# Kernel tuning notes

Hardware: AMD Instinct MI355X
Metric: run time of the kernel (lower is better)

The kernel has to match this reference:

```python
import jax, jax.numpy as jnp
import numpy as np

W_H = 512
RING_WIDTH = 1
IN_F = 128
OUT_F = 128


def _ring_ids():
    # static ring assignment per pixel, mirrors torch module's self.r / ring_width bins
    ax = np.arange(-W_H / 2, W_H / 2, dtype=np.float64)
    x, y = np.meshgrid(ax, ax, indexing='ij')
    r = np.sqrt(x * x + y * y)
    ring = (r // RING_WIDTH).astype(np.int32).reshape(-1)  # [H*W]
    len_r = int(np.sqrt(2.0) * (W_H / 2)) + 1
    iter_r = len_r // RING_WIDTH + (1 if len_r % RING_WIDTH != 0 else 0)
    return jnp.asarray(ring), iter_r


def setup_inputs() -> dict:
    key = jax.random.key(0)
    ks = jax.random.split(key, 7)
    return {
        'image_re': jax.random.normal(ks[0], (W_H, W_H, IN_F), jnp.float32),
        'image_im': jax.random.normal(ks[1], (W_H, W_H, IN_F), jnp.float32),
        'mask': jax.random.randint(ks[2], (W_H, W_H), 0, 2).astype(jnp.int32),
        'output_re': jnp.zeros((W_H, W_H, OUT_F), jnp.float32),
        'output_im': jnp.zeros((W_H, W_H, OUT_F), jnp.float32),
        'w1_re': jax.random.normal(ks[3], (IN_F, OUT_F), jnp.float32),
        'w1_im': jax.random.normal(ks[4], (IN_F, OUT_F), jnp.float32),
        'w2_re': jax.random.normal(ks[5], (IN_F, OUT_F), jnp.float32),
        'w2_im': jax.random.normal(ks[6], (IN_F, OUT_F), jnp.float32),
    }


def reference(image_re, image_im, mask, output_re, output_im,
              w1_re, w1_im, w2_re, w2_im):
    ring, n_rings = _ring_ids()
    H, _, F_in = image_re.shape
    x_re = image_re.reshape(-1, F_in)  # [N, F_in]
    x_im = image_im.reshape(-1, F_in)
    m = mask.reshape(-1, 1)
    u = (m == 0).astype(x_re.dtype)  # uncorrupted indicator
    c = (m == 1).astype(x_re.dtype)  # corrupted indicator

    # uncor complex matmul (x*u) @ W1, as 4 real GEMMs
    xu_re, xu_im = x_re * u, x_im * u
    mm1_re = xu_re @ w1_re - xu_im @ w1_im
    mm1_im = xu_re @ w1_im + xu_im @ w1_re

    # per-ring mean of mm1 (denominator = full ring size, matching neighbor.shape[0])
    counts = jax.ops.segment_sum(jnp.ones((x_re.shape[0],), x_re.dtype), ring,
                                 num_segments=n_rings)
    denom = jnp.maximum(counts, 1.0)[:, None]
    sum_re = jax.ops.segment_sum(mm1_re, ring, num_segments=n_rings) / denom
    sum_im = jax.ops.segment_sum(mm1_im, ring, num_segments=n_rings) / denom
    sre = sum_re[ring]  # [N, F_out] per-pixel broadcast of its ring mean
    sim = sum_im[ring]

    # cor complex matmul (x*c) @ W2
    xc_re, xc_im = x_re * c, x_im * c
    mm2_re = xc_re @ w2_re - xc_im @ w2_im
    mm2_im = xc_re @ w2_im + xc_im @ w2_re

    out_re = u * (0.5 * (mm1_re + sre)) + c * (mm2_re - sre)
    out_im = u * (0.5 * (mm1_im + sim)) + c * (mm2_im - sim)
    # real/imag stacked on last axis -> [H, H, F_out, 2]
    return jnp.stack([out_re, out_im], axis=-1).reshape(H, H, -1, 2)
```

## Files before the change

kernel.cpp:

```cpp
#include <hip/hip_runtime.h>
#include <hip/hip_bf16.h>
#include <stdint.h>


#define WH 512
#define NPIX (WH * WH)
#define NF 128
#define NRINGS 363

typedef unsigned short u16;
typedef __attribute__((ext_vector_type(8))) short short8;
typedef __attribute__((ext_vector_type(4))) float floatx4;

__device__ __forceinline__ u16 f2bf(float x) {
    uint32_t u = __float_as_uint(x);
    uint32_t r = (u + 0x7FFFu + ((u >> 16) & 1u)) >> 16;
    return (u16)r;
}
__device__ __forceinline__ uint32_t pk(float a, float b) {
    return (uint32_t)f2bf(a) | ((uint32_t)f2bf(b) << 16);
}
__device__ __forceinline__ short8 negbf(short8 v) {
    union { short8 s; uint32_t u[4]; } x;
    x.s = v;
    x.u[0] ^= 0x80008000u; x.u[1] ^= 0x80008000u;
    x.u[2] ^= 0x80008000u; x.u[3] ^= 0x80008000u;
    return x.s;
}
__device__ __forceinline__ floatx4 mfma16(short8 a, short8 b, floatx4 c) {
    return __builtin_amdgcn_mfma_f32_16x16x32_bf16(a, b, c, 0, 0, 0);
}

__global__ void k_build_bt(const float* __restrict__ w1r, const float* __restrict__ w1i,
                           const float* __restrict__ w2r, const float* __restrict__ w2i,
                           u16* __restrict__ bt) {
    int n = blockIdx.x, k = threadIdx.x;
    int src = k * NF + n;
    float a1r = w1r[src], a1i = w1i[src], a2r = w2r[src], a2i = w2i[src];
    int d = n * NF + k;
    bt[0 * 16384 + d] = f2bf(a1r - a2r);
    bt[1 * 16384 + d] = f2bf(a2r);
    bt[2 * 16384 + d] = f2bf(a1i - a2i);
    bt[3 * 16384 + d] = f2bf(a2i);
}

#define BROW 40
#define LDS_AR 0
#define LDS_AI 5120
#define LDS_B  10240

__global__ __launch_bounds__(256, 2) void k_gemm(
    const float* __restrict__ xr, const float* __restrict__ xi,
    const int* __restrict__ mask, const u16* __restrict__ bt,
    float* __restrict__ out)
{
    __shared__ u16 lds[30720];
    const int t = threadIdx.x;
    const int pbase = blockIdx.x * 128;
    const int w = t >> 6, lane = t & 63;
    const int quad = lane >> 4, l16 = lane & 15;

    floatx4 accRe[2][8], accIm[2][8];
#pragma unroll
    for (int mi = 0; mi < 2; mi++)
#pragma unroll
        for (int ni = 0; ni < 8; ni++) {
            accRe[mi][ni] = (floatx4)0.0f;
            accIm[mi][ni] = (floatx4)0.0f;
        }

    bool uu[2];
    uu[0] = (mask[pbase + w * 32 + l16] == 0);
    uu[1] = (mask[pbase + w * 32 + 16 + l16] == 0);

    const int sr = t >> 1, sh = t & 1;
    const float4* xr4 = (const float4*)(xr + (size_t)(pbase + sr) * NF);
    const float4* xi4 = (const float4*)(xi + (size_t)(pbase + sr) * NF);

    for (int kw = 0; kw < 4; kw++) {
        if (kw) __syncthreads();
        {
            int qb = kw * 8 + sh * 4;
            float4 r0 = xr4[qb], r1 = xr4[qb + 1], r2 = xr4[qb + 2], r3 = xr4[qb + 3];
            float4 i0 = xi4[qb], i1 = xi4[qb + 1], i2 = xi4[qb + 2], i3 = xi4[qb + 3];
            uint4 a, b;
            a.x = pk(r0.x, r0.y); a.y = pk(r0.z, r0.w); a.z = pk(r1.x, r1.y); a.w = pk(r1.z, r1.w);
            b.x = pk(r2.x, r2.y); b.y = pk(r2.z, r2.w); b.z = pk(r3.x, r3.y); b.w = pk(r3.z, r3.w);
            *(uint4*)&lds[LDS_AR + sr * BROW + sh * 16]     = a;
            *(uint4*)&lds[LDS_AR + sr * BROW + sh * 16 + 8] = b;
            a.x = pk(i0.x, i0.y); a.y = pk(i0.z, i0.w); a.z = pk(i1.x, i1.y); a.w = pk(i1.z, i1.w);
            b.x = pk(i2.x, i2.y); b.y = pk(i2.z, i2.w); b.z = pk(i3.x, i3.y); b.w = pk(i3.z, i3.w);
            *(uint4*)&lds[LDS_AI + sr * BROW + sh * 16]     = a;
            *(uint4*)&lds[LDS_AI + sr * BROW + sh * 16 + 8] = b;
        }
#pragma unroll
        for (int q = 0; q < 8; q++) {
            int fi = q * 256 + t;
            int mat = fi >> 9;
            int wi = fi & 511;
            int n = wi >> 2, kc = wi & 3;
            uint4 v = *(const uint4*)(bt + mat * 16384 + n * 128 + kw * 32 + kc * 8);
            *(uint4*)&lds[LDS_B + mat * 5120 + n * BROW + kc * 8] = v;
        }
        __syncthreads();

        short8 ar[2], ai[2], aru[2], aiu[2];
#pragma unroll
        for (int mi = 0; mi < 2; mi++) {
            int r = w * 32 + mi * 16 + l16;
            ar[mi] = *(short8*)&lds[LDS_AR + r * BROW + quad * 8];
            ai[mi] = *(short8*)&lds[LDS_AI + r * BROW + quad * 8];
            aru[mi] = uu[mi] ? ar[mi] : (short8)0;
            aiu[mi] = uu[mi] ? ai[mi] : (short8)0;
        }
#pragma unroll
        for (int ni = 0; ni < 8; ni++) {
            int nrow = ni * 16 + l16;
            short8 bDr = *(short8*)&lds[LDS_B + 0 * 5120 + nrow * BROW + quad * 8];
            short8 b2r = *(short8*)&lds[LDS_B + 1 * 5120 + nrow * BROW + quad * 8];
            short8 bDi = *(short8*)&lds[LDS_B + 2 * 5120 + nrow * BROW + quad * 8];
            short8 b2i = *(short8*)&lds[LDS_B + 3 * 5120 + nrow * BROW + quad * 8];
            short8 bDin = negbf(bDi), b2in = negbf(b2i);
#pragma unroll
            for (int mi = 0; mi < 2; mi++) {
                accRe[mi][ni] = mfma16(aru[mi], bDr,  accRe[mi][ni]);
                accRe[mi][ni] = mfma16(ar[mi],  b2r,  accRe[mi][ni]);
                accRe[mi][ni] = mfma16(aiu[mi], bDin, accRe[mi][ni]);
                accRe[mi][ni] = mfma16(ai[mi],  b2in, accRe[mi][ni]);
                accIm[mi][ni] = mfma16(aru[mi], bDi,  accIm[mi][ni]);
                accIm[mi][ni] = mfma16(ar[mi],  b2i,  accIm[mi][ni]);
                accIm[mi][ni] = mfma16(aiu[mi], bDr,  accIm[mi][ni]);
                accIm[mi][ni] = mfma16(ai[mi],  b2r,  accIm[mi][ni]);
            }
        }
    }

#pragma unroll
    for (int mi = 0; mi < 2; mi++)
#pragma unroll
        for (int ni = 0; ni < 8; ni++)
#pragma unroll
            for (int r = 0; r < 4; r++) {
                int p = pbase + w * 32 + mi * 16 + quad * 4 + r;
                int f = ni * 16 + l16;
                float2 v;
                v.x = accRe[mi][ni][r];
                v.y = accIm[mi][ni][r];
                *(float2*)(out + (size_t)p * 256 + f * 2) = v;
            }
}

__global__ void k_ringsum(const float* __restrict__ y, const int* __restrict__ mask,
                          float* __restrict__ rs, float* __restrict__ cnt)
{
    const int R = blockIdx.x;
    const int t = threadIdx.x;
    const int row0 = blockIdx.y * 128;
    const int R2 = R * R, R12 = (R + 1) * (R + 1);
    float acc = 0.0f;
    int count = 0;
    for (int i = row0; i < row0 + 128; i++) {
        int x = i - 256;
        int x2 = x * x;
        int hi2 = R12 - x2;
        if (hi2 <= 0) continue;
        int lo2 = R2 - x2;
        int a = 0;
        if (lo2 > 0) {
            a = (int)ceilf(sqrtf((float)lo2));
            while (a * a < lo2) a++;
            while (a > 0 && (a - 1) * (a - 1) >= lo2) a--;
        }
        int b = (int)ceilf(sqrtf((float)hi2));
        while (b * b < hi2) b++;
        while (b > 0 && (b - 1) * (b - 1) >= hi2) b--;
        int yhi = min(b - 1, 255);
        for (int yy = a; yy <= yhi; yy++) {
            int p = i * 512 + (yy + 256);
            count++;
            if (mask[p] == 0) acc += y[(size_t)p * 256 + t];
        }
        int ylo = max(a, 1);
        int yhi2 = min(b - 1, 256);
        for (int yy = ylo; yy <= yhi2; yy++) {
            int p = i * 512 + (256 - yy);
            count++;
            if (mask[p] == 0) acc += y[(size_t)p * 256 + t];
        }
    }
    atomicAdd(&rs[R * 256 + t], acc);
    if (t == 0) atomicAdd(&cnt[R], (float)count);
}

__global__ void k_final(const int* __restrict__ mask, const float* __restrict__ rs,
                        const float* __restrict__ cnt, float* __restrict__ out)
{
    const int t = threadIdx.x;
    const int p0 = blockIdx.x * 64;
    for (int pp = 0; pp < 64; pp++) {
        int p = p0 + pp;
        int i = p >> 9, j = p & 511;
        int x = i - 256, yy = j - 256;
        int r2 = x * x + yy * yy;
        int R = (int)sqrtf((float)r2);
        while ((R + 1) * (R + 1) <= r2) R++;
        while (R * R > r2) R--;
        float c = cnt[R];
        c = (c < 1.0f) ? 1.0f : c;
        float s = rs[R * 256 + t] / c;
        float v = out[(size_t)p * 256 + t];
        float o = (mask[p] == 0) ? 0.5f * (v + s) : (v - s);
        out[(size_t)p * 256 + t] = o;
    }
}

extern "C" void kernel_launch(void* const* d_in, const int* in_sizes, int n_in,
                              void* d_out, int out_size, void* d_ws, size_t ws_size,
                              hipStream_t stream)
{
    const float* xr  = (const float*)d_in[0];
    const float* xi  = (const float*)d_in[1];
    const int*   msk = (const int*)d_in[2];
    const float* w1r = (const float*)d_in[5];
    const float* w1i = (const float*)d_in[6];
    const float* w2r = (const float*)d_in[7];
    const float* w2i = (const float*)d_in[8];
    float* out = (float*)d_out;

    float* rs  = (float*)d_ws;
    float* cnt = rs + NRINGS * 256;
    u16*   bt  = (u16*)((char*)d_ws + 373248);

    hipMemsetAsync(d_ws, 0, (size_t)(NRINGS * 256 + NRINGS) * sizeof(float), stream);
    k_build_bt<<<dim3(128), dim3(128), 0, stream>>>(w1r, w1i, w2r, w2i, bt);
    k_gemm<<<dim3(NPIX / 128), dim3(256), 0, stream>>>(xr, xi, msk, bt, out);
    k_ringsum<<<dim3(NRINGS, 4), dim3(256), 0, stream>>>(out, msk, rs, cnt);
    k_final<<<dim3(NPIX / 64), dim3(256), 0, stream>>>(msk, rs, cnt, out);
}
```

Baseline: 927.3 us.

## Build per-ring pixel index lists for ring-sum reduction instead of geometric scanning

Adds a scatter kernel that assigns each pixel to its ring, counts all ring members, and appends uncorrupted pixel indices to a per-ring list using atomics. The ring-sum kernel then reads only listed pixels in chunks of 128 across a 363x13 grid, replacing per-row sqrt-bound scans and per-pixel mask checks. This aims to spread the ring reduction over more blocks and to drop wasted mask reads. The cost is an extra kernel with global atomics, a larger workspace, and a list order that varies between runs, so the float sums are no longer deterministic.

```diff
diff --git a/kernel.cpp b/kernel.cpp
--- a/kernel.cpp
+++ b/kernel.cpp
@@ -7,6 +7,7 @@
 #define NPIX (WH * WH)
 #define NF 128
 #define NRINGS 363
+#define SLAB 1664
 
 typedef unsigned short u16;
 typedef __attribute__((ext_vector_type(8))) short short8;
@@ -29,6 +30,15 @@
 }
 __device__ __forceinline__ floatx4 mfma16(short8 a, short8 b, floatx4 c) {
     return __builtin_amdgcn_mfma_f32_16x16x32_bf16(a, b, c, 0, 0, 0);
+}
+__device__ __forceinline__ int ring_of(int p) {
+    int i = p >> 9, j = p & 511;
+    int x = i - 256, y = j - 256;
+    int r2 = x * x + y * y;
+    int R = (int)sqrtf((float)r2);
+    while ((R + 1) * (R + 1) <= r2) R++;
+    while (R * R > r2) R--;
+    return R;
 }
 
 __global__ void k_build_bt(const float* __restrict__ w1r, const float* __restrict__ w1i,
@@ -150,62 +160,49 @@
             }
 }
 
-__global__ void k_ringsum(const float* __restrict__ y, const int* __restrict__ mask,
-                          float* __restrict__ rs, float* __restrict__ cnt)
+__global__ void k_scatter(const int* __restrict__ mask, int* __restrict__ ctr,
+                          int* __restrict__ totcnt, int* __restrict__ list)
+{
+    int p = blockIdx.x * 256 + threadIdx.x;
+    int R = ring_of(p);
+    atomicAdd(&totcnt[R], 1);
+    if (mask[p] == 0) {
+        int slot = atomicAdd(&ctr[R], 1);
+        list[R * SLAB + slot] = p;
+    }
+}
+
+__global__ __launch_bounds__(256) void k_ringsum2(
+    const float* __restrict__ y, const int* __restrict__ ctr,
+    const int* __restrict__ list, float* __restrict__ rs)
 {
     const int R = blockIdx.x;
+    const int nu = ctr[R];
+    const int s0 = blockIdx.y * 128;
+    if (s0 >= nu) return;
+    const int n = min(128, nu - s0);
+    __shared__ int sl[128];
     const int t = threadIdx.x;
-    const int row0 = blockIdx.y * 128;
-    const int R2 = R * R, R12 = (R + 1) * (R + 1);
+    if (t < 128) sl[t] = (t < n) ? list[R * SLAB + s0 + t] : 0;
+    __syncthreads();
     float acc = 0.0f;
-    int count = 0;
-    for (int i = row0; i < row0 + 128; i++) {
-        int x = i - 256;
-        int x2 = x * x;
-        int hi2 = R12 - x2;
-        if (hi2 <= 0) continue;
-        int lo2 = R2 - x2;
-        int a = 0;
-        if (lo2 > 0) {
-            a = (int)ceilf(sqrtf((float)lo2));
-            while (a * a < lo2) a++;
-            while (a > 0 && (a - 1) * (a - 1) >= lo2) a--;
-        }
-        int b = (int)ceilf(sqrtf((float)hi2));
-        while (b * b < hi2) b++;
-        while (b > 0 && (b - 1) * (b - 1) >= hi2) b--;
-        int yhi = min(b - 1, 255);
-        for (int yy = a; yy <= yhi; yy++) {
-            int p = i * 512 + (yy + 256);
-            count++;
-            if (mask[p] == 0) acc += y[(size_t)p * 256 + t];
-        }
-        int ylo = max(a, 1);
-        int yhi2 = min(b - 1, 256);
-        for (int yy = ylo; yy <= yhi2; yy++) {
-            int p = i * 512 + (256 - yy);
-            count++;
-            if (mask[p] == 0) acc += y[(size_t)p * 256 + t];
-        }
+#pragma unroll 4
+    for (int k = 0; k < n; k++) {
+        int p = sl[k];
+        acc += y[(size_t)p * 256 + t];
     }
     atomicAdd(&rs[R * 256 + t], acc);
-    if (t == 0) atomicAdd(&cnt[R], (float)count);
 }
 
 __global__ void k_final(const int* __restrict__ mask, const float* __restrict__ rs,
-                        const float* __restrict__ cnt, float* __restrict__ out)
+                        const int* __restrict__ totcnt, float* __restrict__ out)
 {
     const int t = threadIdx.x;
     const int p0 = blockIdx.x * 64;
     for (int pp = 0; pp < 64; pp++) {
         int p = p0 + pp;
-        int i = p >> 9, j = p & 511;
-        int x = i - 256, yy = j - 256;
-        int r2 = x * x + yy * yy;
-        int R = (int)sqrtf((float)r2);
-        while ((R + 1) * (R + 1) <= r2) R++;
-        while (R * R > r2) R--;
-        float c = cnt[R];
+        int R = ring_of(p);
+        float c = (float)totcnt[R];
         c = (c < 1.0f) ? 1.0f : c;
         float s = rs[R * 256 + t] / c;
         float v = out[(size_t)p * 256 + t];
@@ -227,13 +224,17 @@
     const float* w2i = (const float*)d_in[8];
     float* out = (float*)d_out;
 
-    float* rs  = (float*)d_ws;
-    float* cnt = rs + NRINGS * 256;
-    u16*   bt  = (u16*)((char*)d_ws + 373248);
-
-    hipMemsetAsync(d_ws, 0, (size_t)(NRINGS * 256 + NRINGS) * sizeof(float), stream);
+    char* wsb = (char*)d_ws;
+    float* rs     = (float*)(wsb + 0);
+    int*   ctr    = (int*)(wsb + 371712);
+    int*   totcnt = (int*)(wsb + 373248);
+    int*   list   = (int*)(wsb + 374784);
+    u16*   bt     = (u16*)(wsb + 2790912);
+
+    hipMemsetAsync(d_ws, 0, 374784, stream);
     k_build_bt<<<dim3(128), dim3(128), 0, stream>>>(w1r, w1i, w2r, w2i, bt);
     k_gemm<<<dim3(NPIX / 128), dim3(256), 0, stream>>>(xr, xi, msk, bt, out);
-    k_ringsum<<<dim3(NRINGS, 4), dim3(256), 0, stream>>>(out, msk, rs, cnt);
-    k_final<<<dim3(NPIX / 64), dim3(256), 0, stream>>>(msk, rs, cnt, out);
-}
+    k_scatter<<<dim3(NPIX / 256), dim3(256), 0, stream>>>(msk, ctr, totcnt, list);
+    k_ringsum2<<<dim3(NRINGS, 13), dim3(256), 0, stream>>>(out, ctr, list, rs);
+    k_final<<<dim3(NPIX / 64), dim3(256), 0, stream>>>(msk, rs, totcnt, out);
+}
```

Result: faster. 902.1 us (-2.7%).
